# Optimization experiments

Measured on AMD Instinct MI355X. Metric: run time of the kernel, lower is better.

The kernel has to match this reference:

```python
import jax, jax.numpy as jnp
import numpy as np
from jax import lax

BN_EPS = 1e-5
BIG = 1e10


def farthest_point_sample(xyz, S):
    # pytorch3d sample_farthest_points with random_start_point=False: start at index 0
    B, N, _ = xyz.shape

    def step(carry, _):
        min_d, last_idx = carry
        last = jnp.take_along_axis(xyz, last_idx[:, None, None], axis=1)  # [B,1,3]
        d = jnp.sum((xyz - last) ** 2, axis=-1)  # [B,N]
        min_d = jnp.minimum(min_d, d)
        nxt = jnp.argmax(min_d, axis=-1).astype(jnp.int32)
        return (min_d, nxt), last_idx

    init = (jnp.full((B, N), BIG, xyz.dtype), jnp.zeros((B,), jnp.int32))
    _, idxs = lax.scan(step, init, None, length=S)  # [S,B]
    idxs = jnp.swapaxes(idxs, 0, 1)  # [B,S]
    new_xyz = jnp.take_along_axis(xyz, idxs[..., None], axis=1)  # [B,S,3]
    return new_xyz, idxs


def knn_idx(query, pts, K):
    # squared-distance top-k (pytorch3d knn_points uses squared L2)
    d2 = (jnp.sum(query ** 2, -1)[:, :, None]
          + jnp.sum(pts ** 2, -1)[:, None, :]
          - 2.0 * jnp.einsum('bsc,bnc->bsn', query, pts))  # [B,S,N]
    _, idx = lax.top_k(-d2, K)  # [B,S,K], nearest first
    return idx


def knn_gather(x, idx):
    # x: [B,N,C], idx: [B,S,K] -> [B,S,K,C]
    return jax.vmap(lambda pts, i: pts[i])(x, idx)


def batchnorm(x, gamma, beta):
    # x: [B,S,K,C]; training-mode BN: batch stats over (B,S,K), biased variance
    mean = jnp.mean(x, axis=(0, 1, 2))
    var = jnp.mean((x - mean) ** 2, axis=(0, 1, 2))
    return (x - mean) * lax.rsqrt(var + BN_EPS) * gamma + beta


def setup_inputs() -> dict:
    key = jax.random.key(0)
    ks = jax.random.split(key, 4)
    B, N, F, S, K, C = 4, 8192, 64, 2048, 16, 128
    xyz = jax.random.normal(ks[0], (B, N, 3), jnp.float32)
    features = jax.random.normal(ks[1], (B, N, F), jnp.float32)
    w0 = jax.random.normal(ks[2], (C, F + 3), jnp.float32) * (1.0 / np.sqrt(F + 3))
    b0 = jnp.zeros((C,), jnp.float32)
    g0 = jnp.ones((C,), jnp.float32)
    be0 = jnp.zeros((C,), jnp.float32)
    w1 = jax.random.normal(ks[3], (C, C), jnp.float32) * (1.0 / np.sqrt(C))
    b1 = jnp.zeros((C,), jnp.float32)
    g1 = jnp.ones((C,), jnp.float32)
    be1 = jnp.zeros((C,), jnp.float32)
    return {"xyz": xyz, "features": features, "w0": w0, "b0": b0, "g0": g0,
            "be0": be0, "w1": w1, "b1": b1, "g1": g1, "be1": be1}


def reference(xyz, features, w0, b0, g0, be0, w1, b1, g1, be1):
    S, K = 2048, 16
    new_xyz, _ = farthest_point_sample(xyz, S)        # [B,S,3]
    idx = knn_idx(new_xyz, xyz, K)                    # [B,S,K]
    grouped_xyz = knn_gather(xyz, idx)                # [B,S,K,3]
    grouped_xyz_norm = grouped_xyz - new_xyz[:, :, None, :]
    grouped_feat = knn_gather(features, idx)          # [B,S,K,F]
    h = jnp.concatenate([grouped_xyz_norm, grouped_feat], axis=-1)  # [B,S,K,F+3]
    # layer 0: 1x1 conv + BN + ReLU
    h = jnp.einsum('bskc,oc->bsko', h, w0) + b0
    h = jax.nn.relu(batchnorm(h, g0, be0))
    # layer 1
    h = jnp.einsum('bskc,oc->bsko', h, w1) + b1
    h = jax.nn.relu(batchnorm(h, g1, be1))
    new_features = jnp.max(h, axis=2)                 # [B,S,C] max over K
    return new_xyz, new_features
```

## Files before the change

### kernel.cpp

```cpp
#include <hip/hip_runtime.h>

#define B 4
#define N 8192
#define F 64
#define S 2048
#define K 16
#define C 128
#define R (B*S*K)

typedef float v2f __attribute__((ext_vector_type(2)));

__device__ __forceinline__ float norm2f(float x, float y, float z) {
#pragma clang fp contract(off)
  return (x*x + y*y) + z*z;
}

__device__ __forceinline__ float knn_d2(float4 q, float4 p) {
#pragma clang fp contract(off)
  float dot = (q.x*p.x + q.y*p.y) + q.z*p.z;
  return (q.w + p.w) - 2.0f*dot;
}

__device__ __forceinline__ void pinf(float& v) { asm volatile("" : "+v"(v)); }

#define DPP_U(v, ctrl) ((unsigned)__builtin_amdgcn_update_dpp(0, (int)(v), ctrl, 0xf, 0xf, true))
#define DPP_F(v, ctrl) __int_as_float((int)DPP_U(__float_as_uint(v), ctrl))
__device__ __forceinline__ unsigned umaxu(unsigned a, unsigned b) { return a > b ? a : b; }

#define WAVE_MAX_U(x) do { \
  x = umaxu(x, DPP_U(x,0x111)); x = umaxu(x, DPP_U(x,0x112)); \
  x = umaxu(x, DPP_U(x,0x114)); x = umaxu(x, DPP_U(x,0x118)); \
  x = umaxu(x, DPP_U(x,0x142)); x = umaxu(x, DPP_U(x,0x143)); } while(0)

#define WAVE_MAX_F(x) do { \
  x = fmaxf(x, DPP_F(x,0x111)); x = fmaxf(x, DPP_F(x,0x112)); \
  x = fmaxf(x, DPP_F(x,0x114)); x = fmaxf(x, DPP_F(x,0x118)); \
  x = fmaxf(x, DPP_F(x,0x142)); x = fmaxf(x, DPP_F(x,0x143)); } while(0)

__global__ void prep_kernel(const float* __restrict__ xyz, float4* __restrict__ pts4,
                            unsigned* __restrict__ prog) {
  int i = blockIdx.x*blockDim.x + threadIdx.x;
  if (i < B) prog[i] = 0u;
  if (i >= B*N) return;
  float x = xyz[i*3+0], y = xyz[i*3+1], z = xyz[i*3+2];
  pts4[i] = make_float4(x, y, z, norm2f(x, y, z));
}

__global__ void transpose_w1_kernel(const float* __restrict__ w1, float* __restrict__ w1t) {
  int i = blockIdx.x*256 + threadIdx.x;
  int o = i >> 7, c = i & 127;
  w1t[c*C + o] = w1[o*C + c];
}

__global__ __launch_bounds__(256, 1) void fps_knn_kernel(const float4* __restrict__ pts4,
                                                         float4* __restrict__ q4,
                                                         float* __restrict__ out_xyz,
                                                         int* __restrict__ knn,
                                                         unsigned* __restrict__ prog) {
  __shared__ float4 cw[N];
  __shared__ __align__(16) unsigned long long redarr[2][4];

  if (blockIdx.x < B) {
    const int b = blockIdx.x;
    const int t = threadIdx.x;
    const float4* pb = pts4 + b*N;

    v2f px[16], py[16], pz[16], md[16];
#pragma unroll
    for (int j = 0; j < 16; ++j) {
      int i0 = (2*j)*256 + t, i1 = (2*j+1)*256 + t;
      float4 v0 = pb[i0];
      float4 v1 = pb[i1];
      cw[i0] = v0; cw[i1] = v1;
      pinf(v0.x); pinf(v0.y); pinf(v0.z);
      pinf(v1.x); pinf(v1.y); pinf(v1.z);
      px[j] = (v2f){v0.x, v1.x};
      py[j] = (v2f){v0.y, v1.y};
      pz[j] = (v2f){v0.z, v1.z};
      md[j] = (v2f){1e10f, 1e10f};
    }
    __syncthreads();

    float wx, wy, wz;
    { float4 p0 = pb[0]; wx = p0.x; wy = p0.y; wz = p0.z; }

    for (int s = 0; ; ++s) {
      if (t == 0) {
        if ((s & 31) == 0 && s) {
          __threadfence();
          __hip_atomic_store(prog + b, (unsigned)s, __ATOMIC_RELAXED, __HIP_MEMORY_SCOPE_AGENT);
        }
        float w2 = norm2f(wx, wy, wz);
        q4[b*S + s] = make_float4(wx, wy, wz, w2);
      }
      if (s == S-1) break;

      v2f wxx = (v2f){wx, wx}, wyy = (v2f){wy, wy}, wzz = (v2f){wz, wz};
      float bvA = -1.0f, bvB = -1.0f; int biA = 0, biB = 0;
#pragma unroll
      for (int j = 0; j < 16; ++j) {
#pragma clang fp contract(off)
        v2f dx = px[j] - wxx;
        v2f dy = py[j] - wyy;
        v2f dz = pz[j] - wzz;
        v2f d  = (dx*dx + dy*dy) + dz*dz;
        v2f m;
        m.x = fminf(md[j].x, d.x);
        m.y = fminf(md[j].y, d.y);
        md[j] = m;
        if (j < 8) {
          bool g0 = m.x > bvA;  bvA = g0 ? m.x : bvA;  biA = g0 ? (2*j)   : biA;
          bool g1 = m.y > bvA;  bvA = g1 ? m.y : bvA;  biA = g1 ? (2*j+1) : biA;
        } else {
          bool g0 = m.x > bvB;  bvB = g0 ? m.x : bvB;  biB = g0 ? (2*j)   : biB;
          bool g1 = m.y > bvB;  bvB = g1 ? m.y : bvB;  biB = g1 ? (2*j+1) : biB;
        }
      }
      bool gB = bvB > bvA;
      float bv = gB ? bvB : bvA;
      int   bi = gB ? biB : biA;

      float v = bv;
      WAVE_MAX_F(v);
      float wmaxv = __int_as_float(__builtin_amdgcn_readlane(__float_as_int(v), 63));
      unsigned loi = 8191u - (((unsigned)bi << 8) + (unsigned)t);
      unsigned tmp = (bv == wmaxv) ? loi : 0u;
      WAVE_MAX_U(tmp);
      if ((t & 63) == 63)
        redarr[s & 1][t >> 6] = ((unsigned long long)__float_as_uint(wmaxv) << 32)
                              | (unsigned long long)tmp;
      __syncthreads();

      const unsigned long long* ra = redarr[s & 1];
      double k0 = __longlong_as_double((long long)ra[0]);
      double k1 = __longlong_as_double((long long)ra[1]);
      double k2 = __longlong_as_double((long long)ra[2]);
      double k3 = __longlong_as_double((long long)ra[3]);
      double g  = fmax(fmax(k0, k1), fmax(k2, k3));
      unsigned long long gb = (unsigned long long)__double_as_longlong(g);
      int w = 8191 - (int)((unsigned)gb & 0x1FFFu);
      float4 pw = cw[w];
      wx = pw.x; wy = pw.y; wz = pw.z;
    }
    if (t == 0) {
      __threadfence();
      __hip_atomic_store(prog + b, (unsigned)S, __ATOMIC_RELAXED, __HIP_MEMORY_SCOPE_AGENT);
    }
    __syncthreads();
    for (int i = t; i < S; i += 256) {
      float4 v = q4[b*S + i];
      out_xyz[(b*S + i)*3 + 0] = v.x;
      out_xyz[(b*S + i)*3 + 1] = v.y;
      out_xyz[(b*S + i)*3 + 2] = v.z;
    }
  } else {
    const int qw   = (blockIdx.x - B)*4 + (threadIdx.x >> 6);
    const int lane = threadIdx.x & 63;
    const int b    = qw & 3;
    const int s    = qw >> 2;
    const int bs   = b*S + s;
    const float4* pb = pts4 + (size_t)b*N;

    while (__hip_atomic_load(prog + b, __ATOMIC_RELAXED, __HIP_MEMORY_SCOPE_AGENT) <= (unsigned)s)
      __builtin_amdgcn_s_sleep(64);
    __threadfence();

    float4 q = q4[bs];

    float dv[16]; int di[16];
#pragma unroll
    for (int j = 0; j < 16; ++j) { dv[j] = 3.4e38f; di[j] = 0x7FFFFFFF; }

    for (int j = 0; j < N/64; ++j) {
      int n = j*64 + lane;
      float4 p = pb[n];
      float d2 = knn_d2(q, p);
#pragma unroll
      for (int k = 15; k >= 1; --k) {
        bool s1 = d2 < dv[k-1];
        bool s2 = d2 < dv[k];
        dv[k] = fmaxf(dv[k-1], fminf(d2, dv[k]));
        di[k] = s1 ? di[k-1] : (s2 ? n : di[k]);
      }
      bool s0 = d2 < dv[0];
      dv[0] = fminf(d2, dv[0]);
      di[0] = s0 ? n : di[0];
    }

    int myg = 0;
#pragma unroll 1
    for (int r = 0; r < 16; ++r) {
      unsigned bits = __float_as_uint(dv[0]);
      unsigned ord  = bits ^ (0x80000000u | (unsigned)(((int)bits) >> 31));
      unsigned mk   = ~ord;
      unsigned m = mk;
      WAVE_MAX_U(m);
      unsigned wm = (unsigned)__builtin_amdgcn_readlane((int)m, 63);
      unsigned ci = (mk == wm) ? ~(unsigned)di[0] : 0u;
      unsigned m2 = ci;
      WAVE_MAX_U(m2);
      unsigned wi = (unsigned)__builtin_amdgcn_readlane((int)m2, 63);
      int g = (int)~wi;
      if (lane == r) myg = g;
      bool win = (mk == wm) && ((unsigned)di[0] == ~wi);
#pragma unroll
      for (int k = 0; k < 15; ++k) {
        dv[k] = win ? dv[k+1] : dv[k];
        di[k] = win ? di[k+1] : di[k];
      }
      dv[15] = win ? 3.4e38f    : dv[15];
      di[15] = win ? 0x7FFFFFFF : di[15];
    }
    if (lane < 16) knn[bs*16 + lane] = myg;
  }
}

__global__ __launch_bounds__(256, 2) void gemm0_kernel(const float4* __restrict__ pts4,
                                                       const float4* __restrict__ q4,
                                                       const float* __restrict__ feat,
                                                       const int* __restrict__ knn,
                                                       const float* __restrict__ w0,
                                                       const float* __restrict__ b0,
                                                       float* __restrict__ Z) {
  int r = blockIdx.x*256 + threadIdx.x;
  int bs = r >> 4;
  int b  = r >> 15;
  int p  = knn[r];
  float4 q  = q4[bs];
  float4 pp = pts4[b*N + p];

  float row[67];
  row[0] = pp.x - q.x; row[1] = pp.y - q.y; row[2] = pp.z - q.z;
  const float4* fp = (const float4*)(feat + (size_t)(b*N + p)*F);
#pragma unroll
  for (int i = 0; i < 16; ++i) {
    float4 v = fp[i];
    row[3+4*i] = v.x; row[4+4*i] = v.y; row[5+4*i] = v.z; row[6+4*i] = v.w;
  }

  float* zr = Z + (size_t)r*C;
  for (int og = 0; og < C/4; ++og) {
    float a0 = b0[og*4+0], a1 = b0[og*4+1], a2 = b0[og*4+2], a3 = b0[og*4+3];
    const float* wr = w0 + og*4*67;
#pragma unroll
    for (int c = 0; c < 67; ++c) {
      float x = row[c];
      a0 = fmaf(x, wr[c      ], a0);
      a1 = fmaf(x, wr[67  + c], a1);
      a2 = fmaf(x, wr[134 + c], a2);
      a3 = fmaf(x, wr[201 + c], a3);
    }
    ((float4*)zr)[og] = make_float4(a0, a1, a2, a3);
  }
}

__global__ void stats_kernel(const float* __restrict__ Z, float* __restrict__ part) {
  int c = threadIdx.x & 127;
  int g = threadIdx.x >> 7;
  int chunk = blockIdx.x*2 + g;
  const int rows = R/256;
  const float* zp = Z + (size_t)chunk*rows*C + c;
  float s1 = 0.f, s2 = 0.f;
  for (int j = 0; j < rows; ++j) {
    float v = zp[(size_t)j*C];
    s1 += v;
    s2 = fmaf(v, v, s2);
  }
  __shared__ float sh[2][2][128];
  sh[g][0][c] = s1; sh[g][1][c] = s2;
  __syncthreads();
  if (g == 0) {
    part[(blockIdx.x*128 + c)*2 + 0] = s1 + sh[1][0][c];
    part[(blockIdx.x*128 + c)*2 + 1] = s2 + sh[1][1][c];
  }
}

__global__ void finalize_kernel(const float* __restrict__ part,
                                const float* __restrict__ gamma,
                                const float* __restrict__ beta,
                                float* __restrict__ AB) {
  int c = threadIdx.x;
  float s1 = 0.f, s2 = 0.f;
  for (int i = 0; i < 128; ++i) {
    s1 += part[(i*128 + c)*2 + 0];
    s2 += part[(i*128 + c)*2 + 1];
  }
  const float inv = 1.0f/(float)R;
  float mean = s1*inv;
  float var  = s2*inv - mean*mean;
  float rstd = rsqrtf(var + 1e-5f);
  float a = gamma[c]*rstd;
  AB[c]     = a;
  AB[C + c] = beta[c] - mean*a;
}

__global__ __launch_bounds__(256, 4) void gemm1_kernel(float* __restrict__ Z,
                                                       const float* __restrict__ AB0,
                                                       const float* __restrict__ w1t,
                                                       const float* __restrict__ b1) {
  __shared__ float hs[64 * 129];
  const int tid = threadIdx.x;
  const size_t base = (size_t)blockIdx.x * 64;

  const float4* Z4 = (const float4*)(Z + base * C);
#pragma unroll
  for (int k = 0; k < 8; ++k) {
    int f = tid + k*256;
    int row = f >> 5, c4 = f & 31;
    float4 v  = Z4[f];
    float4 A  = ((const float4*)AB0)[c4];
    float4 Bb = ((const float4*)AB0)[32 + c4];
    int lb = row*129 + c4*4;
    hs[lb+0] = fmaxf(fmaf(v.x, A.x, Bb.x), 0.f);
    hs[lb+1] = fmaxf(fmaf(v.y, A.y, Bb.y), 0.f);
    hs[lb+2] = fmaxf(fmaf(v.z, A.z, Bb.z), 0.f);
    hs[lb+3] = fmaxf(fmaf(v.w, A.w, Bb.w), 0.f);
  }
  __syncthreads();

  const int row = tid & 63;
  const int qu  = __builtin_amdgcn_readfirstlane(tid >> 6);
  const float* wq = w1t + qu*32;
  float acc[32];
#pragma unroll
  for (int o = 0; o < 32; ++o) acc[o] = b1[qu*32 + o];
  const float* hrow = hs + row*129;
  for (int c = 0; c < C; ++c) {
    float x = hrow[c];
    const float* wr = wq + c*C;
#pragma unroll
    for (int o = 0; o < 32; ++o) acc[o] = fmaf(x, wr[o], acc[o]);
  }
  __syncthreads();

#pragma unroll
  for (int o = 0; o < 32; ++o) hs[row*129 + qu*32 + o] = acc[o];
  __syncthreads();
  float4* Zo = (float4*)(Z + base * C);
#pragma unroll
  for (int k = 0; k < 8; ++k) {
    int f = tid + k*256;
    int row2 = f >> 5, c4 = f & 31;
    int lb = row2*129 + c4*4;
    Zo[f] = make_float4(hs[lb+0], hs[lb+1], hs[lb+2], hs[lb+3]);
  }
}

__global__ void maxpool_kernel(const float* __restrict__ Z,
                               const float* __restrict__ AB1,
                               float* __restrict__ outF) {
  int t = blockIdx.x*256 + threadIdx.x;
  int bs = t >> 5, c4 = t & 31;
  const float4* zp = (const float4*)Z + (size_t)bs*K*(C/4) + c4;
  float4 A  = ((const float4*)AB1)[c4];
  float4 Bb = ((const float4*)(AB1 + C))[c4];
  float4 m = make_float4(-3.4e38f, -3.4e38f, -3.4e38f, -3.4e38f);
#pragma unroll
  for (int k = 0; k < K; ++k) {
    float4 z = zp[(size_t)k*(C/4)];
    m.x = fmaxf(m.x, fmaf(z.x, A.x, Bb.x));
    m.y = fmaxf(m.y, fmaf(z.y, A.y, Bb.y));
    m.z = fmaxf(m.z, fmaf(z.z, A.z, Bb.z));
    m.w = fmaxf(m.w, fmaf(z.w, A.w, Bb.w));
  }
  m.x = fmaxf(m.x, 0.f); m.y = fmaxf(m.y, 0.f);
  m.z = fmaxf(m.z, 0.f); m.w = fmaxf(m.w, 0.f);
  ((float4*)outF)[t] = m;
}

extern "C" void kernel_launch(void* const* d_in, const int* in_sizes, int n_in,
                              void* d_out, int out_size, void* d_ws, size_t ws_size,
                              hipStream_t stream) {
  const float* xyz      = (const float*)d_in[0];
  const float* features = (const float*)d_in[1];
  const float* w0  = (const float*)d_in[2];
  const float* b0  = (const float*)d_in[3];
  const float* g0  = (const float*)d_in[4];
  const float* be0 = (const float*)d_in[5];
  const float* w1  = (const float*)d_in[6];
  const float* b1  = (const float*)d_in[7];
  const float* g1  = (const float*)d_in[8];
  const float* be1 = (const float*)d_in[9];

  char* wp = (char*)d_ws;
  float4* pts4 = (float4*)wp;  wp += (size_t)B*N*sizeof(float4);
  float4* q4   = (float4*)wp;  wp += (size_t)B*S*sizeof(float4);
  int*    knn  = (int*)wp;     wp += (size_t)R*sizeof(int);
  float*  Z    = (float*)wp;   wp += (size_t)R*C*sizeof(float);
  float*  part = (float*)wp;   wp += (size_t)128*C*2*sizeof(float);
  float*  AB0  = (float*)wp;   wp += (size_t)2*C*sizeof(float);
  float*  AB1  = (float*)wp;   wp += (size_t)2*C*sizeof(float);
  float*  w1t  = (float*)wp;   wp += (size_t)C*C*sizeof(float);
  unsigned* prog = (unsigned*)wp; wp += 4*sizeof(unsigned);

  float* out_xyz  = (float*)d_out;
  float* out_feat = (float*)d_out + B*S*3;

  prep_kernel<<<(B*N)/256, 256, 0, stream>>>(xyz, pts4, prog);
  transpose_w1_kernel<<<(C*C)/256, 256, 0, stream>>>(w1, w1t);
  fps_knn_kernel<<<B + (B*S)/4, 256, 0, stream>>>(pts4, q4, out_xyz, knn, prog);
  gemm0_kernel<<<R/256, 256, 0, stream>>>(pts4, q4, features, knn, w0, b0, Z);
  stats_kernel<<<128, 256, 0, stream>>>(Z, part);
  finalize_kernel<<<1, 128, 0, stream>>>(part, g0, be0, AB0);
  gemm1_kernel<<<R/64, 256, 0, stream>>>(Z, AB0, w1t, b1);
  stats_kernel<<<128, 256, 0, stream>>>(Z, part);
  finalize_kernel<<<1, 128, 0, stream>>>(part, g1, be1, AB1);
  maxpool_kernel<<<(B*S*32)/256, 256, 0, stream>>>(Z, AB1, out_feat);
}
```

Measured before the change: 2.044 ms.

## Fuse layer-0 GEMM into KNN waves and replace FPS barrier with tagged spin

Removes the separate gemm0 kernel and the knn index buffer. Each KNN wave now computes the 1x1 conv layer 0 for its 16 neighbours directly, using a transposed w0 so lanes read weights coalesced, and overlaps this work with the long FPS blocks. The FPS per-step __syncthreads is replaced by volatile LDS tag/key slots that every thread polls, which avoids a full block barrier on each of the 2048 steps. The trade-offs are extra per-wave work with only 2 outputs per lane, and a spin loop that depends on LDS visibility ordering across waves.

Result: slower. 2.841 ms (+39.0%).

```diff
diff --git a/kernel.cpp b/kernel.cpp
--- a/kernel.cpp
+++ b/kernel.cpp
@@ -52,18 +52,31 @@
   w1t[c*C + o] = w1[o*C + c];
 }
 
+__global__ void transpose_w0_kernel(const float* __restrict__ w0, float* __restrict__ w0t) {
+  int i = blockIdx.x*256 + threadIdx.x;
+  if (i >= 67*C) return;
+  int c = i >> 7, o = i & 127;
+  w0t[c*C + o] = w0[o*67 + c];
+}
+
 __global__ __launch_bounds__(256, 1) void fps_knn_kernel(const float4* __restrict__ pts4,
                                                          float4* __restrict__ q4,
                                                          float* __restrict__ out_xyz,
-                                                         int* __restrict__ knn,
+                                                         const float* __restrict__ feat,
+                                                         const float* __restrict__ w0t,
+                                                         const float* __restrict__ b0,
+                                                         float* __restrict__ Z,
                                                          unsigned* __restrict__ prog) {
   __shared__ float4 cw[N];
-  __shared__ __align__(16) unsigned long long redarr[2][4];
+  __shared__ __align__(16) unsigned long long keys[2][4];
+  __shared__ __align__(16) unsigned tags[2][4];
 
   if (blockIdx.x < B) {
     const int b = blockIdx.x;
     const int t = threadIdx.x;
     const float4* pb = pts4 + b*N;
+
+    if (t < 8) ((unsigned*)tags)[t] = 0u;
 
     v2f px[16], py[16], pz[16], md[16];
 #pragma unroll
@@ -126,17 +139,29 @@
       unsigned loi = 8191u - (((unsigned)bi << 8) + (unsigned)t);
       unsigned tmp = (bv == wmaxv) ? loi : 0u;
       WAVE_MAX_U(tmp);
-      if ((t & 63) == 63)
-        redarr[s & 1][t >> 6] = ((unsigned long long)__float_as_uint(wmaxv) << 32)
-                              | (unsigned long long)tmp;
-      __syncthreads();
-
-      const unsigned long long* ra = redarr[s & 1];
-      double k0 = __longlong_as_double((long long)ra[0]);
-      double k1 = __longlong_as_double((long long)ra[1]);
-      double k2 = __longlong_as_double((long long)ra[2]);
-      double k3 = __longlong_as_double((long long)ra[3]);
-      double g  = fmax(fmax(k0, k1), fmax(k2, k3));
+
+      const int par = s & 1;
+      const unsigned su = (unsigned)s + 1u;
+      if ((t & 63) == 63) {
+        *(volatile unsigned long long*)&keys[par][t >> 6] =
+            ((unsigned long long)__float_as_uint(wmaxv) << 32) | (unsigned long long)tmp;
+        *(volatile unsigned*)&tags[par][t >> 6] = su;
+      }
+      unsigned long long k0, k1, k2, k3;
+      {
+        volatile const unsigned* vt = &tags[par][0];
+        volatile const unsigned long long* vk = &keys[par][0];
+        for (;;) {
+          unsigned a0 = vt[0], a1 = vt[1], a2 = vt[2], a3 = vt[3];
+          k0 = vk[0]; k1 = vk[1]; k2 = vk[2]; k3 = vk[3];
+          if (((a0 ^ su) | (a1 ^ su) | (a2 ^ su) | (a3 ^ su)) == 0u) break;
+        }
+      }
+      double d0 = __longlong_as_double((long long)k0);
+      double d1 = __longlong_as_double((long long)k1);
+      double d2 = __longlong_as_double((long long)k2);
+      double d3 = __longlong_as_double((long long)k3);
+      double g  = fmax(fmax(d0, d1), fmax(d2, d3));
       unsigned long long gb = (unsigned long long)__double_as_longlong(g);
       int w = 8191 - (int)((unsigned)gb & 0x1FFFu);
       float4 pw = cw[w];
@@ -211,46 +236,34 @@
       dv[15] = win ? 3.4e38f    : dv[15];
       di[15] = win ? 0x7FFFFFFF : di[15];
     }
-    if (lane < 16) knn[bs*16 + lane] = myg;
-  }
-}
-
-__global__ __launch_bounds__(256, 2) void gemm0_kernel(const float4* __restrict__ pts4,
-                                                       const float4* __restrict__ q4,
-                                                       const float* __restrict__ feat,
-                                                       const int* __restrict__ knn,
-                                                       const float* __restrict__ w0,
-                                                       const float* __restrict__ b0,
-                                                       float* __restrict__ Z) {
-  int r = blockIdx.x*256 + threadIdx.x;
-  int bs = r >> 4;
-  int b  = r >> 15;
-  int p  = knn[r];
-  float4 q  = q4[bs];
-  float4 pp = pts4[b*N + p];
-
-  float row[67];
-  row[0] = pp.x - q.x; row[1] = pp.y - q.y; row[2] = pp.z - q.z;
-  const float4* fp = (const float4*)(feat + (size_t)(b*N + p)*F);
-#pragma unroll
-  for (int i = 0; i < 16; ++i) {
-    float4 v = fp[i];
-    row[3+4*i] = v.x; row[4+4*i] = v.y; row[5+4*i] = v.z; row[6+4*i] = v.w;
-  }
-
-  float* zr = Z + (size_t)r*C;
-  for (int og = 0; og < C/4; ++og) {
-    float a0 = b0[og*4+0], a1 = b0[og*4+1], a2 = b0[og*4+2], a3 = b0[og*4+3];
-    const float* wr = w0 + og*4*67;
-#pragma unroll
-    for (int c = 0; c < 67; ++c) {
-      float x = row[c];
-      a0 = fmaf(x, wr[c      ], a0);
-      a1 = fmaf(x, wr[67  + c], a1);
-      a2 = fmaf(x, wr[134 + c], a2);
-      a3 = fmaf(x, wr[201 + c], a3);
-    }
-    ((float4*)zr)[og] = make_float4(a0, a1, a2, a3);
+
+    const int o0 = lane;
+    const float bb0 = b0[o0];
+    const float bb1 = b0[o0 + 64];
+    const float* w0c = w0t + o0;
+    float* zb = Z + (size_t)bs*K*C;
+#pragma unroll 1
+    for (int k = 0; k < K; ++k) {
+      int p = __builtin_amdgcn_readlane(myg, k);
+      float4 pp = pts4[(size_t)b*N + p];
+      float a0 = bb0, a1 = bb1;
+      float x0 = pp.x - q.x, x1 = pp.y - q.y, x2 = pp.z - q.z;
+      a0 = fmaf(x0, w0c[0*C],      a0); a1 = fmaf(x0, w0c[0*C + 64], a1);
+      a0 = fmaf(x1, w0c[1*C],      a0); a1 = fmaf(x1, w0c[1*C + 64], a1);
+      a0 = fmaf(x2, w0c[2*C],      a0); a1 = fmaf(x2, w0c[2*C + 64], a1);
+      const float4* fp = (const float4*)(feat + ((size_t)b*N + p)*F);
+#pragma unroll
+      for (int i = 0; i < 16; ++i) {
+        float4 vv = fp[i];
+        const float* wc = w0c + (3 + 4*i)*C;
+        a0 = fmaf(vv.x, wc[0*C], a0); a1 = fmaf(vv.x, wc[0*C + 64], a1);
+        a0 = fmaf(vv.y, wc[1*C], a0); a1 = fmaf(vv.y, wc[1*C + 64], a1);
+        a0 = fmaf(vv.z, wc[2*C], a0); a1 = fmaf(vv.z, wc[2*C + 64], a1);
+        a0 = fmaf(vv.w, wc[3*C], a0); a1 = fmaf(vv.w, wc[3*C + 64], a1);
+      }
+      zb[k*C + o0]      = a0;
+      zb[k*C + o0 + 64] = a1;
+    }
   }
 }
 
@@ -385,12 +398,12 @@
   char* wp = (char*)d_ws;
   float4* pts4 = (float4*)wp;  wp += (size_t)B*N*sizeof(float4);
   float4* q4   = (float4*)wp;  wp += (size_t)B*S*sizeof(float4);
-  int*    knn  = (int*)wp;     wp += (size_t)R*sizeof(int);
   float*  Z    = (float*)wp;   wp += (size_t)R*C*sizeof(float);
   float*  part = (float*)wp;   wp += (size_t)128*C*2*sizeof(float);
   float*  AB0  = (float*)wp;   wp += (size_t)2*C*sizeof(float);
   float*  AB1  = (float*)wp;   wp += (size_t)2*C*sizeof(float);
   float*  w1t  = (float*)wp;   wp += (size_t)C*C*sizeof(float);
+  float*  w0t  = (float*)wp;   wp += (size_t)67*C*sizeof(float);
   unsigned* prog = (unsigned*)wp; wp += 4*sizeof(unsigned);
 
   float* out_xyz  = (float*)d_out;
@@ -398,8 +411,8 @@
 
   prep_kernel<<<(B*N)/256, 256, 0, stream>>>(xyz, pts4, prog);
   transpose_w1_kernel<<<(C*C)/256, 256, 0, stream>>>(w1, w1t);
-  fps_knn_kernel<<<B + (B*S)/4, 256, 0, stream>>>(pts4, q4, out_xyz, knn, prog);
-  gemm0_kernel<<<R/256, 256, 0, stream>>>(pts4, q4, features, knn, w0, b0, Z);
+  transpose_w0_kernel<<<34, 256, 0, stream>>>(w0, w0t);
+  fps_knn_kernel<<<B + (B*S)/4, 256, 0, stream>>>(pts4, q4, out_xyz, features, w0t, b0, Z, prog);
   stats_kernel<<<128, 256, 0, stream>>>(Z, part);
   finalize_kernel<<<1, 128, 0, stream>>>(part, g0, be0, AB0);
   gemm1_kernel<<<R/64, 256, 0, stream>>>(Z, AB0, w1t, b1);
```
